# Kernel tuning notes

Measured on AMD Instinct MI355X. Metric: run time of the kernel, lower is better.

The kernel has to match this reference:

```python
import jax, jax.numpy as jnp
import numpy as np
from jax import lax

HID = 128  # hidden_dim
K = 2      # kernel (must be 2 for the torch slice arithmetic to be shape-consistent)


def skew(x):
    # x: (B,C,H,W) -> (B,C,H,2W-1), row r shifted right by r
    B, C, H, W = x.shape
    rows = jnp.arange(H)[:, None]
    cols = jnp.arange(W)[None, :] + rows
    y = jnp.zeros((B, C, H, 2 * W - 1), x.dtype)
    return y.at[:, :, rows, cols].set(x)


def unskew(x):
    B, C, H, Wp = x.shape
    W = (Wp + 1) // 2
    rows = jnp.arange(H)[:, None]
    cols = jnp.arange(W)[None, :] + rows
    return x[:, :, rows, cols]


def setup_inputs() -> dict:
    key = jax.random.key(0)
    k1, k2, k3 = jax.random.split(key, 3)
    Cin = 128
    x = jax.random.normal(k1, (8, Cin, 64, 64), jnp.float32)
    w_is = jax.random.normal(k2, (4 * HID, Cin), jnp.float32) * 0.05   # 1x1 conv weight
    b_is = jnp.zeros((4 * HID,), jnp.float32)
    w_ss = jax.random.normal(k3, (4 * HID, HID, K, 1), jnp.float32) * 0.05  # (k,1) conv weight
    b_ss = jnp.zeros((4 * HID,), jnp.float32)
    return {"x": x, "w_is": w_is, "b_is": b_is, "w_ss": w_ss, "b_ss": b_ss}


def reference(x, w_is, b_is, w_ss, b_ss):
    B, Cin, H, W = x.shape
    hid, k = HID, K
    xs = skew(x)  # (B,Cin,H,2W-1)
    # input-to-state: 1x1 conv (mask B on 1x1 kernel == plain 1x1 conv)
    z_is = jnp.einsum('bchw,oc->bohw', xs, w_is) + b_is[None, :, None, None]
    steps = z_is.transpose(3, 0, 1, 2)  # (2W-1, B, 4hid, H)

    h0 = jnp.zeros((B, hid, H), x.dtype)
    c0 = jnp.zeros((B, hid, H), x.dtype)

    def step(carry, z_t):
        h, c = carry  # (B,hid,H)
        # state-to-state (k,1) conv along H, padding k//2, then drop last k-1 rows
        hs = lax.conv_general_dilated(h[..., None], w_ss, (1, 1),
                                      [(k // 2, k // 2), (0, 0)],
                                      dimension_numbers=('NCHW', 'OIHW', 'NCHW'))
        hs = hs[:, :, :-(k - 1), 0] + b_ss[None, :, None]  # (B,4hid,H)
        z = z_t + hs
        i = jax.nn.sigmoid(z[:, :hid])
        f = jax.nn.sigmoid(z[:, hid:2 * hid])
        o = jax.nn.sigmoid(z[:, 2 * hid:3 * hid])
        g = jnp.tanh(z[:, 3 * hid:])
        c = f * c + i * g
        h = o * jnp.tanh(c)
        return (h, c), h

    _, hs_all = lax.scan(step, (h0, c0), steps)  # (2W-1,B,hid,H)
    out = hs_all.transpose(1, 2, 3, 0)  # (B,hid,H,2W-1)
    return unskew(out)  # (B,hid,H,W)
```

## Files before the change

### kernel.cpp

```cpp
#include <hip/hip_runtime.h>
#include <hip/hip_fp16.h>
#include <math.h>


#define HID 128
#define BB 8
#define HH 64
#define WW 64
#define TT 127

typedef _Float16 v8h __attribute__((ext_vector_type(8)));
typedef float v4f __attribute__((ext_vector_type(4)));

#define SENT64 0xFFFFFFFFFFFFFFFFULL

__device__ __forceinline__ float fsig(float x) {
  float e = __builtin_amdgcn_exp2f(x * -1.44269504f);
  return __builtin_amdgcn_rcpf(1.f + e);
}
__device__ __forceinline__ float ftanh_(float x) {
  float e = __builtin_amdgcn_exp2f(x * 2.88539009f);
  return __builtin_fmaf(-2.f, __builtin_amdgcn_rcpf(1.f + e), 1.f);
}

__global__ __launch_bounds__(256) void prep_w2(const float* __restrict__ w_ss,
                                               const float* __restrict__ w_is,
                                               const float* __restrict__ b_is,
                                               const float* __restrict__ b_ss,
                                               _Float16* __restrict__ wp,
                                               _Float16* __restrict__ wisa,
                                               __half* __restrict__ zph,
                                               float* __restrict__ bsum512,
                                               unsigned long long* __restrict__ hx) {
  int idx = blockIdx.x * 256 + threadIdx.x;
  if (idx < 131072) {
    int j = idx & 7;
    int L = (idx >> 3) & 63;
    int kt = (idx >> 9) & 7;
    int mt = idx >> 12;
    int O = mt * 16 + (L & 15);
    int k = kt * 32 + ((L >> 4) & 3) * 8 + j;
    float v = (k < 128) ? w_ss[(size_t)O * 256 + k * 2]
                        : w_ss[(size_t)O * 256 + (k - 128) * 2 + 1];
    wp[idx] = (_Float16)v;
  } else if (idx < 196608) {
    int i2 = idx - 131072;
    int j = i2 & 7;
    int L = (i2 >> 3) & 63;
    int kt = (i2 >> 9) & 3;
    int mt = i2 >> 11;
    int O = mt * 16 + (L & 15);
    int k = kt * 32 + ((L >> 4) & 3) * 8 + j;
    wisa[i2] = (_Float16)w_is[(size_t)O * 128 + k];
  } else if (idx < 197120) {
    int idx2 = idx - 196608;
    int g = (idx2 >> 2) & 3;
    int u = (idx2 >> 4) * 4 + (idx2 & 3);
    int O = g * 128 + u;
    zph[(size_t)BB * HH * WW * 512 + idx2] = __float2half(b_is[O] + b_ss[O]);
  } else if (idx < 197632) {
    int O = idx - 197120;
    bsum512[O] = b_is[O] + b_ss[O];
  } else if (idx < 197632 + 130048) {
    int j = idx - 197632;
    uint4 s;
    s.x = 0xFFFFFFFFu;
    s.y = 0xFFFFFFFFu;
    s.z = 0xFFFFFFFFu;
    s.w = 0xFFFFFFFFu;
    ((uint4*)hx)[j] = s;
  }
}

__global__ __launch_bounds__(256) void zpre_mfma(const float* __restrict__ x,
                                                 const _Float16* __restrict__ wisa,
                                                 const float* __restrict__ bsum512,
                                                 __half* __restrict__ zph) {
  const int b = blockIdx.x >> 6;
  const int r = blockIdx.x & 63;
  const int tid = threadIdx.x;
  const int wv = tid >> 6;
  const int L = tid & 63;
  const int quad = L >> 4;
  const int l15 = L & 15;

  __shared__ _Float16 xt[64][136];
  __shared__ float bs[512];

  if (tid < 128) {
    *(float4*)&bs[tid * 4] = *(const float4*)&bsum512[tid * 4];
  }
  {
    const int cw = tid >> 4;
    const int w4 = (tid & 15) * 4;
#pragma unroll
    for (int p = 0; p < 8; p++) {
      int c = p * 16 + cw;
      float4 v = *(const float4*)&x[(((size_t)b * 128 + c) * HH + r) * WW + w4];
      xt[w4 + 0][c] = (_Float16)v.x;
      xt[w4 + 1][c] = (_Float16)v.y;
      xt[w4 + 2][c] = (_Float16)v.z;
      xt[w4 + 3][c] = (_Float16)v.w;
    }
  }
  __syncthreads();

  const int wcol = wv * 16 + l15;
  v8h bf[4];
#pragma unroll
  for (int kt = 0; kt < 4; kt++)
    bf[kt] = *(const v8h*)&xt[wcol][kt * 32 + quad * 8];

  const size_t pos = ((size_t)b * HH + r) * WW + wcol;
  const v8h* wa8 = (const v8h*)wisa;

#pragma unroll 4
  for (int mt = 0; mt < 32; mt++) {
    v4f acc = (v4f){0.f, 0.f, 0.f, 0.f};
#pragma unroll
    for (int kt = 0; kt < 4; kt++) {
      v8h af = wa8[((size_t)mt * 4 + kt) * 64 + L];
      acc = __builtin_amdgcn_mfma_f32_16x16x32_f16(af, bf[kt], acc, 0, 0, 0);
    }
    float4 bv = *(float4*)&bs[mt * 16 + quad * 4];
    __half2 lo = __floats2half2_rn(acc[0] + bv.x, acc[1] + bv.y);
    __half2 hi = __floats2half2_rn(acc[2] + bv.z, acc[3] + bv.w);
    uint2 pk;
    pk.x = *(unsigned*)&lo;
    pk.y = *(unsigned*)&hi;
    *(uint2*)&zph[pos * 512 + ((mt & 7) * 4 + quad) * 16 + (mt >> 3) * 4] = pk;
  }
}

#define HROW 136

#define STEP_BARRIER()                                   \
  do {                                                   \
    asm volatile("s_waitcnt lgkmcnt(0)" ::: "memory");   \
    __builtin_amdgcn_s_barrier();                        \
    asm volatile("" ::: "memory");                       \
  } while (0)

#define STEP_BODY(T, RB)                                                       \
  do {                                                                         \
           \
    v8h bfr[4];                                                                \
    _Pragma("unroll") for (int kt = 0; kt < 4; kt++)                           \
        bfr[kt] = *(const v8h*)&h_lds[RB][(rl * 2 + bl) * HROW + kt * 32 +     \
                                          quad * 8];                           \
                  \
    unsigned long long newp = 0ull;                                            \
    if (is_cons && (T) + 1 < TT)                                               \
      newp = __hip_atomic_load(ca + 2048, __ATOMIC_RELAXED,                    \
                               __HIP_MEMORY_SCOPE_AGENT);                      \
           \
    float zf[16];                                                              \
    _Pragma("unroll") for (int i = 0; i < 16; i++)                             \
        zf[i] = __half2float(zu.h[i]);                                         \
         \
    {                                                                          \
      const uint4* p = (const uint4*)(((unsigned)wn < WW) ? zcur : zbias);     \
      zu.q[0] = p[0];                                                          \
      zu.q[1] = p[1];                                                          \
      wn++;                                                                    \
      zcur += 512;                                                             \
    }                                                                          \
             \
    v4f acc0[4], acc1[4];                                                      \
    _Pragma("unroll") for (int g = 0; g < 4; g++) {                            \
      acc0[g] = (v4f){0.f, 0.f, 0.f, 0.f};                                     \
      acc1[g] = (v4f){0.f, 0.f, 0.f, 0.f};                                     \
    }                                                                          \
    _Pragma("unroll") for (int kt = 0; kt < 4; kt++) {                         \
      _Pragma("unroll") for (int g = 0; g < 4; g++)                            \
          acc0[g] = __builtin_amdgcn_mfma_f32_16x16x32_f16(                    \
              wfrag[g][kt], bfr[kt], acc0[g], 0, 0, 0);                        \
    }                                                                          \
    _Pragma("unroll") for (int kt = 0; kt < 4; kt++) {                         \
      v8h bf1 = *(const v8h*)&h_lds[RB][((rl + 1) * 2 + bl) * HROW + kt * 32 + \
                                        quad * 8];                             \
      _Pragma("unroll") for (int g = 0; g < 4; g++)                            \
          acc1[g] = __builtin_amdgcn_mfma_f32_16x16x32_f16(                    \
              wfrag[g][4 + kt], bf1, acc1[g], 0, 0, 0);                        \
    }                                                                          \
                                      \
    const int w = (T)-r;                                                       \
    const bool inband = ((unsigned)w < WW);                                    \
    float hv[4];                                                               \
    _Pragma("unroll") for (int rg2 = 0; rg2 < 4; rg2++) {                      \
      float z0 = (acc0[0][rg2] + acc1[0][rg2]) + zf[0 * 4 + rg2];              \
      float z1 = (acc0[1][rg2] + acc1[1][rg2]) + zf[1 * 4 + rg2];              \
      float z2 = (acc0[2][rg2] + acc1[2][rg2]) + zf[2 * 4 + rg2];              \
      float z3 = (acc0[3][rg2] + acc1[3][rg2]) + zf[3 * 4 + rg2];              \
      float iv = fsig(z0);                                                     \
      float fv = fsig(z1);                                                     \
      float ov = fsig(z2);                                                     \
      float gv = ftanh_(z3);                                                   \
      c[rg2] = fv * c[rg2] + iv * gv;                                          \
      hv[rg2] = ov * ftanh_(c[rg2]);                                           \
    }                                                                          \
                       \
    __half2 plo = __floats2half2_rn(hv[0], hv[1]);                             \
    __half2 phi = __floats2half2_rn(hv[2], hv[3]);                             \
    {                                                                          \
      uint2 pk;                                                                \
      pk.x = *(unsigned*)&plo;                                                 \
      pk.y = *(unsigned*)&phi;                                                 \
      *(uint2*)&h_lds[(RB) ^ 1][((rl + 1) * 2 + bl) * HROW + uq0] = pk;        \
    }                                                                          \
              \
    if (rgr < 7 && l15 >= 14) {                                                \
      unsigned long long pk =                                                  \
          ((unsigned long long)*(unsigned*)&phi << 32) | *(unsigned*)&plo;     \
      __hip_atomic_store(pa, pk, __ATOMIC_RELAXED, __HIP_MEMORY_SCOPE_AGENT);  \
    }                                                                          \
    pa += 2048;                                                                \
             \
    _Pragma("unroll") for (int rg2 = 0; rg2 < 4; rg2++) {                      \
      outb[rg2].x = outb[rg2].y;                                               \
      outb[rg2].y = outb[rg2].z;                                               \
      outb[rg2].z = outb[rg2].w;                                               \
      outb[rg2].w = hv[rg2];                                                   \
    }                                                                          \
    if (inband && (w & 3) == 3) {                                              \
      *(float4*)op0 = outb[0];                                                 \
      *(float4*)op1 = outb[1];                                                 \
      *(float4*)op2 = outb[2];                                                 \
      *(float4*)op3 = outb[3];                                                 \
      op0 += 4;                                                                \
      op1 += 4;                                                                \
      op2 += 4;                                                                \
      op3 += 4;                                                                \
    }                                                                          \
       \
    if (is_cons) {                                                             \
      while (__ballot(pend == SENT64) != 0ull) {                               \
        __builtin_amdgcn_s_sleep(1);                                           \
        pend = __hip_atomic_load(ca, __ATOMIC_RELAXED,                         \
                                 __HIP_MEMORY_SCOPE_AGENT);                    \
      }                                                                        \
      *(unsigned long long*)&h_lds[(RB) ^ 1][(0 * 2 + ebl) * HROW + eu] =      \
          pend;                                                                \
      pend = newp;                                                             \
    }                                                                          \
    ca += 2048;                                                                \
    STEP_BARRIER();                                                            \
  } while (0)

__global__ __launch_bounds__(512, 1) void lstm_mfma(
    const __half* __restrict__ zph, const _Float16* __restrict__ wp,
    unsigned long long* __restrict__ hx,
    float* __restrict__ out) {
  const int blk = blockIdx.x;
  const int rgr = blk >> 2;
  const int bg = blk & 3;
  const int R0 = rgr * 8;
  const int tid = threadIdx.x;
  const int wv = tid >> 6;
  const int L = tid & 63;
  const int quad = L >> 4;
  const int l15 = L & 15;
  const int rl = l15 >> 1;
  const int bl = l15 & 1;
  const int b = bg * 2 + bl;
  const int r = R0 + rl;
  const int uq0 = 16 * wv + quad * 4;
  const int zoff = (4 * wv + quad) * 16;

  __shared__ _Float16 h_lds[2][9 * 2 * HROW];
  for (int i = tid; i < (2 * 9 * 2 * HROW) / 2; i += 512)
    ((unsigned*)h_lds)[i] = 0u;

  v8h wfrag[4][8];
  {
    const v8h* wp8 = (const v8h*)wp;
#pragma unroll
    for (int g = 0; g < 4; g++)
#pragma unroll
      for (int kt = 0; kt < 8; kt++)
        wfrag[g][kt] = wp8[((size_t)((8 * g + wv) * 8 + kt)) * 64 + L];
  }

  float c[4] = {0.f, 0.f, 0.f, 0.f};
  float4 outb[4];
#pragma unroll
  for (int i = 0; i < 4; i++) outb[i] = make_float4(0.f, 0.f, 0.f, 0.f);

  const int ebl = L >> 5;
  const int eu = (L & 31) * 4;
  const int exp_idx = bl * 32 + 4 * wv + quad;

  const bool is_cons = (wv == 0) && (rgr > 0);

  const __half* zpp = zph + ((size_t)b * HH + r) * WW * 512 + zoff;
  const __half* zbias = zph + (size_t)BB * HH * WW * 512 + zoff;
  const unsigned long long* ca =
      hx + (((size_t)(rgr > 0 ? rgr - 1 : 0) * 4 + bg) * 64 + L);
  unsigned long long* pa = hx + (((size_t)rgr * 4 + bg) * 64 + exp_idx);
  float* op0 = out + (((size_t)b * HID + uq0 + 0) * HH + r) * WW;
  float* op1 = out + (((size_t)b * HID + uq0 + 1) * HH + r) * WW;
  float* op2 = out + (((size_t)b * HID + uq0 + 2) * HH + r) * WW;
  float* op3 = out + (((size_t)b * HID + uq0 + 3) * HH + r) * WW;

  union ZU {
    uint4 q[2];
    __half h[16];
  } zu;
  {
    const uint4* p0 = (const uint4*)((r == 0) ? zpp : zbias);
    zu.q[0] = p0[0];
    zu.q[1] = p0[1];
  }
  int wn = 1 - r;
  const __half* zcur = zpp + (ptrdiff_t)wn * 512;

  unsigned long long pend = 0ull;
  if (is_cons) {
    pend = __hip_atomic_load(ca, __ATOMIC_RELAXED, __HIP_MEMORY_SCOPE_AGENT);
  }

  __syncthreads();

  for (int t = 0; t < TT - 1; t += 2) {
    STEP_BODY(t, 0);
    STEP_BODY(t + 1, 1);
  }
  STEP_BODY(TT - 1, 0);
}

__global__ __launch_bounds__(256) void transpose_x(const float* __restrict__ x,
                                                   float* __restrict__ xT) {
  int b = blockIdx.x >> 6;
  int r = blockIdx.x & 63;
  __shared__ float tile[32][65];
  for (int cc = 0; cc < 4; cc++) {
    int cl = threadIdx.x >> 6;
    int w = threadIdx.x & 63;
#pragma unroll
    for (int k = 0; k < 8; k++) {
      int c_loc = k * 4 + cl;
      int c = cc * 32 + c_loc;
      tile[c_loc][w] = x[(((size_t)b * 128 + c) * HH + r) * WW + w];
    }
    __syncthreads();
    int cs = threadIdx.x & 31;
    int wp = threadIdx.x >> 5;
#pragma unroll
    for (int k = 0; k < 8; k++) {
      int w2 = wp * 8 + k;
      xT[(((size_t)b * HH + r) * WW + w2) * 128 + cc * 32 + cs] = tile[cs][w2];
    }
    __syncthreads();
  }
}

__global__ __launch_bounds__(256) void step_kernel(
    const float* __restrict__ x, const float* __restrict__ xT, int use_xT,
    const float* __restrict__ w_is, const float* __restrict__ b_is,
    const float* __restrict__ w_ss, const float* __restrict__ b_ss,
    const float* __restrict__ h_prev, float* __restrict__ h_next,
    float* __restrict__ c_state, float* __restrict__ out, int t) {
  const int rg = blockIdx.x;
  const int q = blockIdx.y;
  const int r0 = rg * 2;
  const int tid = threadIdx.x;
  const int o_loc = tid & 63;
  const int k4 = tid >> 6;
  const int g_ = o_loc >> 4;
  const int u_ = o_loc & 15;
  const int O = g_ * 128 + q * 16 + u_;
  const int i0 = k4 * 32;

  __shared__ __align__(16) float h_in[3][BB][HID];
  __shared__ float zred[16][4][65];

  for (int idx = tid; idx < 3 * BB * HID; idx += 256) {
    int row_sel = idx >> 10;
    int rem = idx & 1023;
    int b = rem >> 7;
    int u = rem & 127;
    int rr = r0 - 1 + row_sel;
    h_in[row_sel][b][u] = (rr >= 0) ? h_prev[((size_t)b * HH + rr) * HID + u] : 0.0f;
  }

  float wr0[32], wr1[32], wz[32];
  {
    const float4* wss4 = (const float4*)(w_ss + ((size_t)O * 128 + i0) * 2);
#pragma unroll
    for (int j = 0; j < 16; j++) {
      float4 v = wss4[j];
      wr0[2 * j] = v.x;
      wr1[2 * j] = v.y;
      wr0[2 * j + 1] = v.z;
      wr1[2 * j + 1] = v.w;
    }
    const float4* wis4 = (const float4*)(w_is + (size_t)O * 128 + i0);
#pragma unroll
    for (int j = 0; j < 8; j++) {
      float4 v = wis4[j];
      wz[4 * j] = v.x;
      wz[4 * j + 1] = v.y;
      wz[4 * j + 2] = v.z;
      wz[4 * j + 3] = v.w;
    }
  }

  __syncthreads();

  float acc[2][BB];
#pragma unroll
  for (int rl = 0; rl < 2; rl++)
#pragma unroll
    for (int b = 0; b < BB; b++) acc[rl][b] = 0.0f;

#pragma unroll
  for (int jb = 0; jb < 8; jb++) {
    int ib = i0 + jb * 4;
#pragma unroll
    for (int b = 0; b < BB; b++) {
      const float4 hm4 = *(const float4*)&h_in[0][b][ib];
      const float4 hc4 = *(const float4*)&h_in[1][b][ib];
      const float4 hp4 = *(const float4*)&h_in[2][b][ib];
      const float* hm = (const float*)&hm4;
      const float* hc = (const float*)&hc4;
      const float* hq = (const float*)&hp4;
#pragma unroll
      for (int jj = 0; jj < 4; jj++) {
        float w0v = wr0[jb * 4 + jj];
        float w1v = wr1[jb * 4 + jj];
        acc[0][b] += w0v * hm[jj] + w1v * hc[jj];
        acc[1][b] += w0v * hc[jj] + w1v * hq[jj];
      }
    }
  }

#pragma unroll
  for (int rl = 0; rl < 2; rl++) {
    int rr = r0 + rl;
    int wcol = t - rr;
    if (wcol >= 0 && wcol < WW) {
      if (use_xT) {
        for (int b = 0; b < BB; b++) {
          const float4* xp =
              (const float4*)(xT + (((size_t)b * HH + rr) * WW + wcol) * 128 + i0);
#pragma unroll
          for (int j = 0; j < 8; j++) {
            float4 v = xp[j];
            acc[rl][b] += wz[4 * j] * v.x + wz[4 * j + 1] * v.y +
                          wz[4 * j + 2] * v.z + wz[4 * j + 3] * v.w;
          }
        }
      } else {
        for (int b = 0; b < BB; b++) {
          const float* xb = x + (((size_t)b * 128 + i0) * HH + rr) * WW + wcol;
#pragma unroll
          for (int j = 0; j < 32; j++) {
            acc[rl][b] += wz[j] * xb[(size_t)j * HH * WW];
          }
        }
      }
    }
  }

#pragma unroll
  for (int rl = 0; rl < 2; rl++)
#pragma unroll
    for (int b = 0; b < BB; b++) zred[rl * 8 + b][k4][o_loc] = acc[rl][b];
  __syncthreads();

  {
    int u = tid >> 4;
    int cell = tid & 15;
    int rl = cell >> 3;
    int b = cell & 7;
    int rr = r0 + rl;
    float z[4];
#pragma unroll
    for (int gg = 0; gg < 4; gg++) {
      int ol = gg * 16 + u;
      float s = zred[cell][0][ol] + zred[cell][1][ol] + zred[cell][2][ol] +
                zred[cell][3][ol];
      int Og = gg * 128 + q * 16 + u;
      z[gg] = s + b_is[Og] + b_ss[Og];
    }
    float iv = 1.0f / (1.0f + expf(-z[0]));
    float fv = 1.0f / (1.0f + expf(-z[1]));
    float ov = 1.0f / (1.0f + expf(-z[2]));
    float gv = tanhf(z[3]);
    int U = q * 16 + u;
    size_t sidx = ((size_t)b * HH + rr) * HID + U;
    float cv = c_state[sidx];
    float cn = fv * cv + iv * gv;
    c_state[sidx] = cn;
    float hn = ov * tanhf(cn);
    h_next[sidx] = hn;
    int wcol = t - rr;
    if (wcol >= 0 && wcol < WW) {
      out[(((size_t)b * HID + U) * HH + rr) * WW + wcol] = hn;
    }
  }
}

extern "C" void kernel_launch(void* const* d_in, const int* in_sizes, int n_in,
                              void* d_out, int out_size, void* d_ws,
                              size_t ws_size, hipStream_t stream) {
  const float* x = (const float*)d_in[0];
  const float* w_is = (const float*)d_in[1];
  const float* b_is = (const float*)d_in[2];
  const float* w_ss = (const float*)d_in[3];
  const float* b_ss = (const float*)d_in[4];
  float* outp = (float*)d_out;

  const size_t zph_bytes = ((size_t)BB * HH * WW * 512 + 512) * 2;
  const size_t wp_bytes = (size_t)512 * 256 * 2;
  const size_t wisa_bytes = (size_t)512 * 128 * 2;
  const size_t hx_bytes = (size_t)TT * 8 * 4 * 64 * 8;
  const size_t bsum_bytes = 512 * sizeof(float);
  const size_t need = zph_bytes + wp_bytes + wisa_bytes + hx_bytes + bsum_bytes;

  char* ws = (char*)d_ws;
  if (ws_size >= need) {
    __half* zph = (__half*)ws;
    _Float16* wpp = (_Float16*)(ws + zph_bytes);
    _Float16* wisa = (_Float16*)(ws + zph_bytes + wp_bytes);
    unsigned long long* hx =
        (unsigned long long*)(ws + zph_bytes + wp_bytes + wisa_bytes);
    float* bsum512 =
        (float*)(ws + zph_bytes + wp_bytes + wisa_bytes + hx_bytes);

    prep_w2<<<dim3(1280), 256, 0, stream>>>(w_ss, w_is, b_is, b_ss, wpp, wisa,
                                            zph, bsum512, hx);
    zpre_mfma<<<dim3(BB * HH), 256, 0, stream>>>(x, wisa, bsum512, zph);
    lstm_mfma<<<dim3(32), 512, 0, stream>>>(zph, wpp, hx, outp);
  } else {
    const size_t xT_elems = (size_t)BB * HH * WW * 128;
    const size_t st_elems = (size_t)BB * HH * HID;
    const size_t need_xT = (xT_elems + 3 * st_elems) * sizeof(float);
    float* wsf = (float*)d_ws;
    float* xT = nullptr;
    float* st;
    int use_xT = 0;
    if (ws_size >= need_xT) {
      use_xT = 1;
      xT = wsf;
      st = wsf + xT_elems;
    } else {
      st = wsf;
    }
    float* h0 = st;
    float* h1 = st + st_elems;
    float* cb = st + 2 * st_elems;
    hipMemsetAsync(st, 0, 3 * st_elems * sizeof(float), stream);
    if (use_xT) transpose_x<<<dim3(BB * HH), 256, 0, stream>>>(x, xT);
    for (int t = 0; t < TT; t++) {
      float* hp = (t & 1) ? h1 : h0;
      float* hn = (t & 1) ? h0 : h1;
      step_kernel<<<dim3(32, 8), 256, 0, stream>>>(x, xT, use_xT, w_is, b_is,
                                                   w_ss, b_ss, hp, hn, cb, outp,
                                                   t);
    }
  }
}
```

Measured before the change: 321.4 us.

## Fuse weight prep into input-projection kernel and seed MFMA accumulators with z

Merges the weight/bias preparation kernel and the input-to-state MFMA projection into one launch, with the projection blocks converting w_is to fp16 fragments directly from global memory and holding them in registers, which removes the wisa and bsum buffers. The projection loop is restructured so each wave keeps 8 M-tiles of weights resident and iterates over 4 column tiles, instead of streaming the weights per tile. In the recurrent step, the precomputed z values are loaded into the second MFMA accumulator as its initial value, which removes separate adds. This trades one kernel launch and some global traffic for higher register pressure in the projection blocks.

```diff
diff --git a/kernel.cpp b/kernel.cpp
--- a/kernel.cpp
+++ b/kernel.cpp
@@ -9,6 +9,8 @@
 #define WW 64
 #define TT 127
 
+#define NPREP 1022
+
 typedef _Float16 v8h __attribute__((ext_vector_type(8)));
 typedef float v4f __attribute__((ext_vector_type(4)));
 
@@ -23,73 +25,54 @@
   return __builtin_fmaf(-2.f, __builtin_amdgcn_rcpf(1.f + e), 1.f);
 }
 
-__global__ __launch_bounds__(256) void prep_w2(const float* __restrict__ w_ss,
-                                               const float* __restrict__ w_is,
-                                               const float* __restrict__ b_is,
-                                               const float* __restrict__ b_ss,
-                                               _Float16* __restrict__ wp,
-                                               _Float16* __restrict__ wisa,
-                                               __half* __restrict__ zph,
-                                               float* __restrict__ bsum512,
-                                               unsigned long long* __restrict__ hx) {
-  int idx = blockIdx.x * 256 + threadIdx.x;
-  if (idx < 131072) {
-    int j = idx & 7;
-    int L = (idx >> 3) & 63;
-    int kt = (idx >> 9) & 7;
-    int mt = idx >> 12;
-    int O = mt * 16 + (L & 15);
-    int k = kt * 32 + ((L >> 4) & 3) * 8 + j;
-    float v = (k < 128) ? w_ss[(size_t)O * 256 + k * 2]
-                        : w_ss[(size_t)O * 256 + (k - 128) * 2 + 1];
-    wp[idx] = (_Float16)v;
-  } else if (idx < 196608) {
-    int i2 = idx - 131072;
-    int j = i2 & 7;
-    int L = (i2 >> 3) & 63;
-    int kt = (i2 >> 9) & 3;
-    int mt = i2 >> 11;
-    int O = mt * 16 + (L & 15);
-    int k = kt * 32 + ((L >> 4) & 3) * 8 + j;
-    wisa[i2] = (_Float16)w_is[(size_t)O * 128 + k];
-  } else if (idx < 197120) {
-    int idx2 = idx - 196608;
-    int g = (idx2 >> 2) & 3;
-    int u = (idx2 >> 4) * 4 + (idx2 & 3);
-    int O = g * 128 + u;
-    zph[(size_t)BB * HH * WW * 512 + idx2] = __float2half(b_is[O] + b_ss[O]);
-  } else if (idx < 197632) {
-    int O = idx - 197120;
-    bsum512[O] = b_is[O] + b_ss[O];
-  } else if (idx < 197632 + 130048) {
-    int j = idx - 197632;
-    uint4 s;
-    s.x = 0xFFFFFFFFu;
-    s.y = 0xFFFFFFFFu;
-    s.z = 0xFFFFFFFFu;
-    s.w = 0xFFFFFFFFu;
-    ((uint4*)hx)[j] = s;
-  }
-}
-
-__global__ __launch_bounds__(256) void zpre_mfma(const float* __restrict__ x,
-                                                 const _Float16* __restrict__ wisa,
-                                                 const float* __restrict__ bsum512,
-                                                 __half* __restrict__ zph) {
-  const int b = blockIdx.x >> 6;
-  const int r = blockIdx.x & 63;
+__global__ __launch_bounds__(256) void prep_zpre(
+    const float* __restrict__ x, const float* __restrict__ w_is,
+    const float* __restrict__ b_is, const float* __restrict__ b_ss,
+    const float* __restrict__ w_ss, _Float16* __restrict__ wp,
+    __half* __restrict__ zph, unsigned long long* __restrict__ hx) {
+  const int bid = blockIdx.x;
   const int tid = threadIdx.x;
+
+  __shared__ _Float16 xt[64][136];
+
+  if (bid < NPREP) {
+    int idx = bid * 256 + tid;
+    if (idx < 131072) {
+      int j = idx & 7;
+      int L = (idx >> 3) & 63;
+      int kt = (idx >> 9) & 7;
+      int mt = idx >> 12;
+      int O = mt * 16 + (L & 15);
+      int k = kt * 32 + ((L >> 4) & 3) * 8 + j;
+      float v = (k < 128) ? w_ss[(size_t)O * 256 + k * 2]
+                          : w_ss[(size_t)O * 256 + (k - 128) * 2 + 1];
+      wp[idx] = (_Float16)v;
+    } else if (idx < 131584) {
+      int idx2 = idx - 131072;
+      int g = (idx2 >> 2) & 3;
+      int u = (idx2 >> 4) * 4 + (idx2 & 3);
+      int O = g * 128 + u;
+      zph[(size_t)BB * HH * WW * 512 + idx2] = __float2half(b_is[O] + b_ss[O]);
+    } else {
+      int j = idx - 131584;
+      uint4 s;
+      s.x = 0xFFFFFFFFu;
+      s.y = 0xFFFFFFFFu;
+      s.z = 0xFFFFFFFFu;
+      s.w = 0xFFFFFFFFu;
+      ((uint4*)hx)[j] = s;
+    }
+    return;
+  }
+
+  const int zb = bid - NPREP;
+  const int b = zb >> 6;
+  const int r = zb & 63;
   const int wv = tid >> 6;
   const int L = tid & 63;
   const int quad = L >> 4;
   const int l15 = L & 15;
 
-  __shared__ _Float16 xt[64][136];
-  __shared__ float bs[512];
-
-  if (tid < 128) {
-    *(float4*)&bs[tid * 4] = *(const float4*)&bsum512[tid * 4];
-  }
   {
     const int cw = tid >> 4;
     const int w4 = (tid & 15) * 4;
@@ -103,32 +86,59 @@
       xt[w4 + 3][c] = (_Float16)v.w;
     }
   }
+
+  v8h wfr[8][4];
+  float4 bv[8];
+#pragma unroll
+  for (int m = 0; m < 8; m++) {
+    const int mt = 8 * wv + m;
+    const int O = mt * 16 + l15;
+#pragma unroll
+    for (int kt = 0; kt < 4; kt++) {
+      const float* p = w_is + (size_t)O * 128 + kt * 32 + quad * 8;
+      float4 a = *(const float4*)p;
+      float4 b2 = *(const float4*)(p + 4);
+      v8h f;
+      f[0] = (_Float16)a.x;
+      f[1] = (_Float16)a.y;
+      f[2] = (_Float16)a.z;
+      f[3] = (_Float16)a.w;
+      f[4] = (_Float16)b2.x;
+      f[5] = (_Float16)b2.y;
+      f[6] = (_Float16)b2.z;
+      f[7] = (_Float16)b2.w;
+      wfr[m][kt] = f;
+    }
+    const int O4 = mt * 16 + quad * 4;
+    float4 bi = *(const float4*)&b_is[O4];
+    float4 bs4 = *(const float4*)&b_ss[O4];
+    bv[m] = make_float4(bi.x + bs4.x, bi.y + bs4.y, bi.z + bs4.z, bi.w + bs4.w);
+  }
+
   __syncthreads();
 
-  const int wcol = wv * 16 + l15;
-  v8h bf[4];
-#pragma unroll
-  for (int kt = 0; kt < 4; kt++)
-    bf[kt] = *(const v8h*)&xt[wcol][kt * 32 + quad * 8];
-
-  const size_t pos = ((size_t)b * HH + r) * WW + wcol;
-  const v8h* wa8 = (const v8h*)wisa;
-
-#pragma unroll 4
-  for (int mt = 0; mt < 32; mt++) {
-    v4f acc = (v4f){0.f, 0.f, 0.f, 0.f};
-#pragma unroll
-    for (int kt = 0; kt < 4; kt++) {
-      v8h af = wa8[((size_t)mt * 4 + kt) * 64 + L];
-      acc = __builtin_amdgcn_mfma_f32_16x16x32_f16(af, bf[kt], acc, 0, 0, 0);
-    }
-    float4 bv = *(float4*)&bs[mt * 16 + quad * 4];
-    __half2 lo = __floats2half2_rn(acc[0] + bv.x, acc[1] + bv.y);
-    __half2 hi = __floats2half2_rn(acc[2] + bv.z, acc[3] + bv.w);
-    uint2 pk;
-    pk.x = *(unsigned*)&lo;
-    pk.y = *(unsigned*)&hi;
-    *(uint2*)&zph[pos * 512 + ((mt & 7) * 4 + quad) * 16 + (mt >> 3) * 4] = pk;
+#pragma unroll
+  for (int nt = 0; nt < 4; nt++) {
+    v8h bf[4];
+#pragma unroll
+    for (int kt = 0; kt < 4; kt++)
+      bf[kt] = *(const v8h*)&xt[nt * 16 + l15][kt * 32 + quad * 8];
+    const size_t pos = ((size_t)b * HH + r) * WW + nt * 16 + l15;
+#pragma unroll
+    for (int m = 0; m < 8; m++) {
+      v4f acc = (v4f){0.f, 0.f, 0.f, 0.f};
+#pragma unroll
+      for (int kt = 0; kt < 4; kt++)
+        acc = __builtin_amdgcn_mfma_f32_16x16x32_f16(wfr[m][kt], bf[kt], acc,
+                                                     0, 0, 0);
+      const int mt = 8 * wv + m;
+      __half2 lo = __floats2half2_rn(acc[0] + bv[m].x, acc[1] + bv[m].y);
+      __half2 hi = __floats2half2_rn(acc[2] + bv[m].z, acc[3] + bv[m].w);
+      uint2 pk;
+      pk.x = *(unsigned*)&lo;
+      pk.y = *(unsigned*)&hi;
+      *(uint2*)&zph[pos * 512 + (m * 4 + quad) * 16 + wv * 4] = pk;
+    }
   }
 }
 
@@ -148,15 +158,16 @@
     _Pragma("unroll") for (int kt = 0; kt < 4; kt++)                           \
         bfr[kt] = *(const v8h*)&h_lds[RB][(rl * 2 + bl) * HROW + kt * 32 +     \
                                           quad * 8];                           \
+         \
+    v4f zi[4];                                                                 \
+    _Pragma("unroll") for (int g = 0; g < 4; g++)                              \
+        _Pragma("unroll") for (int i = 0; i < 4; i++)                          \
+        zi[g][i] = __half2float(zu.h[g * 4 + i]);                              \
                   \
     unsigned long long newp = 0ull;                                            \
     if (is_cons && (T) + 1 < TT)                                               \
       newp = __hip_atomic_load(ca + 2048, __ATOMIC_RELAXED,                    \
                                __HIP_MEMORY_SCOPE_AGENT);                      \
-           \
-    float zf[16];                                                              \
-    _Pragma("unroll") for (int i = 0; i < 16; i++)                             \
-        zf[i] = __half2float(zu.h[i]);                                         \
          \
     {                                                                          \
       const uint4* p = (const uint4*)(((unsigned)wn < WW) ? zcur : zbias);     \
@@ -165,11 +176,11 @@
       wn++;                                                                    \
       zcur += 512;                                                             \
     }                                                                          \
-             \
+          \
     v4f acc0[4], acc1[4];                                                      \
     _Pragma("unroll") for (int g = 0; g < 4; g++) {                            \
       acc0[g] = (v4f){0.f, 0.f, 0.f, 0.f};                                     \
-      acc1[g] = (v4f){0.f, 0.f, 0.f, 0.f};                                     \
+      acc1[g] = zi[g];                                                         \
     }                                                                          \
     _Pragma("unroll") for (int kt = 0; kt < 4; kt++) {                         \
       _Pragma("unroll") for (int g = 0; g < 4; g++)                            \
@@ -183,15 +194,15 @@
           acc1[g] = __builtin_amdgcn_mfma_f32_16x16x32_f16(                    \
               wfrag[g][4 + kt], bf1, acc1[g], 0, 0, 0);                        \
     }                                                                          \
-                                      \
+                        \
     const int w = (T)-r;                                                       \
     const bool inband = ((unsigned)w < WW);                                    \
     float hv[4];                                                               \
     _Pragma("unroll") for (int rg2 = 0; rg2 < 4; rg2++) {                      \
-      float z0 = (acc0[0][rg2] + acc1[0][rg2]) + zf[0 * 4 + rg2];              \
-      float z1 = (acc0[1][rg2] + acc1[1][rg2]) + zf[1 * 4 + rg2];              \
-      float z2 = (acc0[2][rg2] + acc1[2][rg2]) + zf[2 * 4 + rg2];              \
-      float z3 = (acc0[3][rg2] + acc1[3][rg2]) + zf[3 * 4 + rg2];              \
+      float z0 = acc0[0][rg2] + acc1[0][rg2];                                  \
+      float z1 = acc0[1][rg2] + acc1[1][rg2];                                  \
+      float z2 = acc0[2][rg2] + acc1[2][rg2];                                  \
+      float z3 = acc0[3][rg2] + acc1[3][rg2];                                  \
       float iv = fsig(z0);                                                     \
       float fv = fsig(z1);                                                     \
       float ov = fsig(z2);                                                     \
@@ -232,7 +243,7 @@
       op2 += 4;                                                                \
       op3 += 4;                                                                \
     }                                                                          \
-       \
+              \
     if (is_cons) {                                                             \
       while (__ballot(pend == SENT64) != 0ull) {                               \
         __builtin_amdgcn_s_sleep(1);                                           \
@@ -513,24 +524,18 @@
 
   const size_t zph_bytes = ((size_t)BB * HH * WW * 512 + 512) * 2;
   const size_t wp_bytes = (size_t)512 * 256 * 2;
-  const size_t wisa_bytes = (size_t)512 * 128 * 2;
   const size_t hx_bytes = (size_t)TT * 8 * 4 * 64 * 8;
-  const size_t bsum_bytes = 512 * sizeof(float);
-  const size_t need = zph_bytes + wp_bytes + wisa_bytes + hx_bytes + bsum_bytes;
+  const size_t need = zph_bytes + wp_bytes + hx_bytes;
 
   char* ws = (char*)d_ws;
   if (ws_size >= need) {
     __half* zph = (__half*)ws;
     _Float16* wpp = (_Float16*)(ws + zph_bytes);
-    _Float16* wisa = (_Float16*)(ws + zph_bytes + wp_bytes);
     unsigned long long* hx =
-        (unsigned long long*)(ws + zph_bytes + wp_bytes + wisa_bytes);
-    float* bsum512 =
-        (float*)(ws + zph_bytes + wp_bytes + wisa_bytes + hx_bytes);
-
-    prep_w2<<<dim3(1280), 256, 0, stream>>>(w_ss, w_is, b_is, b_ss, wpp, wisa,
-                                            zph, bsum512, hx);
-    zpre_mfma<<<dim3(BB * HH), 256, 0, stream>>>(x, wisa, bsum512, zph);
+        (unsigned long long*)(ws + zph_bytes + wp_bytes);
+
+    prep_zpre<<<dim3(NPREP + 512), 256, 0, stream>>>(x, w_is, b_is, b_ss,
+                                                     w_ss, wpp, zph, hx);
     lstm_mfma<<<dim3(32), 512, 0, stream>>>(zph, wpp, hx, outp);
   } else {
     const size_t xT_elems = (size_t)BB * HH * WW * 128;
```

New measurement: 313.9 us. 2.3% less time.
